# Performance work log

Measured on AMD Instinct MI355X. Metric: run time of the kernel, lower is better.

Reference implementation:

```python
import jax, jax.numpy as jnp
import numpy as np

PAD_VAL = -10000.0


def setup_inputs() -> dict:
    key = jax.random.key(0)
    k1, k2 = jax.random.split(key)
    B, C, H, W = 16, 3, 256, 256
    predicted = jax.random.normal(k1, (B, C, H, W), dtype=jnp.float32)
    ground_truth = jax.random.normal(k2, (B, C, H, W), dtype=jnp.float32)
    return {"predicted": predicted, "ground_truth": ground_truth, "nh": 5, "nw": 5}


def reference(predicted, ground_truth, nh, nw):
    # Faithful to torch: ConstantPad2d((v_pad, v_pad, h_pad, h_pad)) pads
    # W by v_pad = nh//2 and H by h_pad = nw//2 (symmetric when nh == nw).
    v_pad = nh // 2
    h_pad = nw // 2
    B, C, H, W = ground_truth.shape
    gt_pad = jnp.pad(
        ground_truth,
        ((0, 0), (0, 0), (h_pad, h_pad), (v_pad, v_pad)),
        constant_values=PAD_VAL,
    )
    # nh*nw shifted views of the padded ground truth: [B, C, H, W, nh*nw]
    refs = jnp.stack(
        [gt_pad[:, :, i:i + H, j:j + W] for i in range(nh) for j in range(nw)],
        axis=-1,
    )
    # L1 distance over channels for each neighbor shift: [B, H, W, nh*nw]
    norms = jnp.sum(jnp.abs(refs - predicted[..., None]), axis=1)
    # min over neighborhood, then mean over batch/spatial
    return jnp.mean(jnp.min(norms, axis=-1))
```

## Files before the change

kernel.cpp:

```cpp
#include <hip/hip_runtime.h>
#include <math.h>

#define PAD_VAL (-10000.0f)

constexpr int Cc = 3, Hh = 256, Ww = 256, Bb = 16;
constexpr int TW = 64;
constexpr int TH = 16;
constexpr int LDSH = TH + 4;
constexpr int LDSW = 76;
constexpr int F4_PER_ROW = 18;
constexpr int NSLOT = Cc * LDSH * F4_PER_ROW;
constexpr int NTHR  = 128;
constexpr int NBLK  = (Ww / TW) * (Hh / TH) * Bb;


__global__ __launch_bounds__(NTHR) void nnloss_main(
    const float* __restrict__ pred, const float* __restrict__ gt,
    float* __restrict__ partial)
{
    __shared__ float sh[Cc][LDSH][LDSW];
    __shared__ float wsum[2];

    const int bx = blockIdx.x, by = blockIdx.y, b = blockIdx.z;
    const int cbase = bx * TW, rbase = by * TH;
    const int tid = threadIdx.x;
    const size_t base = (size_t)b * Cc * Hh * Ww;

    const int gx  = tid & 15;
    const int ty  = tid >> 4;
    const int pr0 = 2 * ty;
    const int w0  = cbase + 4 * gx;
    const int r0  = rbase + pr0;

    float p[Cc][2][4];
#pragma unroll
    for (int ch = 0; ch < Cc; ++ch)
#pragma unroll
        for (int rr = 0; rr < 2; ++rr) {
            float4 a = *reinterpret_cast<const float4*>(
                &pred[base + ((size_t)ch * Hh + r0 + rr) * Ww + w0]);
            p[ch][rr][0] = a.x; p[ch][rr][1] = a.y;
            p[ch][rr][2] = a.z; p[ch][rr][3] = a.w;
        }

#pragma unroll
    for (int it = 0; it < 9; ++it) {
        int s = tid + it * NTHR;
        if (s < NSLOT) {
            int ch  = s / (LDSH * F4_PER_ROW);
            int rem = s - ch * (LDSH * F4_PER_ROW);
            int lr  = rem / F4_PER_ROW;
            int lc4 = rem - lr * F4_PER_ROW;
            int r   = rbase + lr - 2;
            int c0  = cbase + lc4 * 4 - 4;
            float4 v = make_float4(PAD_VAL, PAD_VAL, PAD_VAL, PAD_VAL);
            if (((unsigned)r < (unsigned)Hh) & ((unsigned)c0 < (unsigned)Ww))
                v = *reinterpret_cast<const float4*>(
                    &gt[base + ((size_t)ch * Hh + r) * Ww + c0]);
            *reinterpret_cast<float4*>(&sh[ch][lr][lc4 * 4]) = v;
        }
    }
    __syncthreads();

    float best[2][4];
#pragma unroll
    for (int rr = 0; rr < 2; ++rr)
#pragma unroll
        for (int px = 0; px < 4; ++px) best[rr][px] = 3.0e38f;

#pragma unroll
    for (int dr = 0; dr < 6; ++dr) {
        float wr[Cc][12];
#pragma unroll
        for (int ch = 0; ch < Cc; ++ch) {
            const float4* q = reinterpret_cast<const float4*>(&sh[ch][pr0 + dr][4 * gx]);
            float4 q0 = q[0], q1 = q[1], q2 = q[2];
            wr[ch][0] = q0.x; wr[ch][1]  = q0.y; wr[ch][2]  = q0.z; wr[ch][3]  = q0.w;
            wr[ch][4] = q1.x; wr[ch][5]  = q1.y; wr[ch][6]  = q1.z; wr[ch][7]  = q1.w;
            wr[ch][8] = q2.x; wr[ch][9]  = q2.y; wr[ch][10] = q2.z; wr[ch][11] = q2.w;
        }
#pragma unroll
        for (int rr = 0; rr < 2; ++rr) {
            if ((rr == 0 && dr <= 4) || (rr == 1 && dr >= 1)) {
#pragma unroll
                for (int dj = 0; dj < 5; ++dj)
#pragma unroll
                    for (int px = 0; px < 4; ++px) {
                        float s = fabsf(wr[0][px + dj + 2] - p[0][rr][px])
                                + fabsf(wr[1][px + dj + 2] - p[1][rr][px])
                                + fabsf(wr[2][px + dj + 2] - p[2][rr][px]);
                        best[rr][px] = fminf(best[rr][px], s);
                    }
            }
        }
    }

    float t = ((best[0][0] + best[0][1]) + (best[0][2] + best[0][3]))
            + ((best[1][0] + best[1][1]) + (best[1][2] + best[1][3]));
#pragma unroll
    for (int off = 32; off; off >>= 1) t += __shfl_down(t, off, 64);
    if ((tid & 63) == 0) wsum[tid >> 6] = t;
    __syncthreads();
    if (tid == 0) {
        int pid = (blockIdx.z * gridDim.y + blockIdx.y) * gridDim.x + blockIdx.x;
        partial[pid] = wsum[0] + wsum[1];
    }
}

__global__ __launch_bounds__(256) void nnloss_reduce(
    const float* __restrict__ partial, int n, float* __restrict__ out)
{
    __shared__ float ws[4];
    float t = 0.0f;
    for (int i = threadIdx.x; i < n; i += 256) t += partial[i];
#pragma unroll
    for (int off = 32; off; off >>= 1) t += __shfl_down(t, off, 64);
    if ((threadIdx.x & 63) == 0) ws[threadIdx.x >> 6] = t;
    __syncthreads();
    if (threadIdx.x == 0)
        out[0] = ((ws[0] + ws[1]) + (ws[2] + ws[3]))
               * (1.0f / ((float)Bb * (float)Hh * (float)Ww));
}

extern "C" void kernel_launch(void* const* d_in, const int* in_sizes, int n_in,
                              void* d_out, int out_size, void* d_ws, size_t ws_size,
                              hipStream_t stream) {
    const float* pred = (const float*)d_in[0];
    const float* gt   = (const float*)d_in[1];
    float* out     = (float*)d_out;
    float* partial = (float*)d_ws;

    dim3 grid(Ww / TW, Hh / TH, Bb);
    nnloss_main<<<grid, NTHR, 0, stream>>>(pred, gt, partial);
    nnloss_reduce<<<1, 256, 0, stream>>>(partial, NBLK, out);
}
```

Measured before the change: 16.90 us.

## Fuse final reduction into main kernel via last-block atomics, halve tile height

Removes the separate reduction kernel launch. The last block to finish, found through per-group and global atomic counters, now sums the partials and writes the mean. The tile height drops from 16 to 8 rows, with one output row per thread, and launch bounds request 4 blocks per CU, giving more and lighter blocks. The counters live in the workspace and rely on modulo wraparound, so results are only correct if the workspace starts zeroed. Smaller tiles also reload more halo rows per block.

```diff
diff --git a/kernel.cpp b/kernel.cpp
--- a/kernel.cpp
+++ b/kernel.cpp
@@ -4,22 +4,25 @@
 #define PAD_VAL (-10000.0f)
 
 constexpr int Cc = 3, Hh = 256, Ww = 256, Bb = 16;
-constexpr int TW = 64;
-constexpr int TH = 16;
+constexpr int TW = 64, TH = 8;
 constexpr int LDSH = TH + 4;
 constexpr int LDSW = 76;
-constexpr int F4_PER_ROW = 18;
-constexpr int NSLOT = Cc * LDSH * F4_PER_ROW;
+constexpr int F4R  = 18;
+constexpr int NSLOT = Cc * LDSH * F4R;
 constexpr int NTHR  = 128;
 constexpr int NBLK  = (Ww / TW) * (Hh / TH) * Bb;
+constexpr int GRP   = 32;
+constexpr int NGRP  = NBLK / GRP;
 
 
-__global__ __launch_bounds__(NTHR) void nnloss_main(
+__global__ __launch_bounds__(NTHR, 4) void nnloss_main(
     const float* __restrict__ pred, const float* __restrict__ gt,
-    float* __restrict__ partial)
+    float* __restrict__ partial, unsigned* __restrict__ gctr,
+    unsigned* __restrict__ fctr, float* __restrict__ out)
 {
     __shared__ float sh[Cc][LDSH][LDSW];
     __shared__ float wsum[2];
+    __shared__ int lastFlag;
 
     const int bx = blockIdx.x, by = blockIdx.y, b = blockIdx.z;
     const int cbase = bx * TW, rbase = by * TH;
@@ -28,29 +31,25 @@
 
     const int gx  = tid & 15;
     const int ty  = tid >> 4;
-    const int pr0 = 2 * ty;
     const int w0  = cbase + 4 * gx;
-    const int r0  = rbase + pr0;
+    const int row = rbase + ty;
 
-    float p[Cc][2][4];
+    float p[Cc][4];
 #pragma unroll
-    for (int ch = 0; ch < Cc; ++ch)
-#pragma unroll
-        for (int rr = 0; rr < 2; ++rr) {
-            float4 a = *reinterpret_cast<const float4*>(
-                &pred[base + ((size_t)ch * Hh + r0 + rr) * Ww + w0]);
-            p[ch][rr][0] = a.x; p[ch][rr][1] = a.y;
-            p[ch][rr][2] = a.z; p[ch][rr][3] = a.w;
-        }
+    for (int ch = 0; ch < Cc; ++ch) {
+        float4 a = *reinterpret_cast<const float4*>(
+            &pred[base + ((size_t)ch * Hh + row) * Ww + w0]);
+        p[ch][0] = a.x; p[ch][1] = a.y; p[ch][2] = a.z; p[ch][3] = a.w;
+    }
 
 #pragma unroll
-    for (int it = 0; it < 9; ++it) {
+    for (int it = 0; it < 6; ++it) {
         int s = tid + it * NTHR;
         if (s < NSLOT) {
-            int ch  = s / (LDSH * F4_PER_ROW);
-            int rem = s - ch * (LDSH * F4_PER_ROW);
-            int lr  = rem / F4_PER_ROW;
-            int lc4 = rem - lr * F4_PER_ROW;
+            int ch  = s / (LDSH * F4R);
+            int rem = s - ch * (LDSH * F4R);
+            int lr  = rem / F4R;
+            int lc4 = rem - lr * F4R;
             int r   = rbase + lr - 2;
             int c0  = cbase + lc4 * 4 - 4;
             float4 v = make_float4(PAD_VAL, PAD_VAL, PAD_VAL, PAD_VAL);
@@ -62,64 +61,67 @@
     }
     __syncthreads();
 
-    float best[2][4];
+    float best[4];
 #pragma unroll
-    for (int rr = 0; rr < 2; ++rr)
-#pragma unroll
-        for (int px = 0; px < 4; ++px) best[rr][px] = 3.0e38f;
+    for (int px = 0; px < 4; ++px) best[px] = 3.0e38f;
 
 #pragma unroll
-    for (int dr = 0; dr < 6; ++dr) {
+    for (int di = 0; di < 5; ++di) {
         float wr[Cc][12];
 #pragma unroll
         for (int ch = 0; ch < Cc; ++ch) {
-            const float4* q = reinterpret_cast<const float4*>(&sh[ch][pr0 + dr][4 * gx]);
+            const float4* q = reinterpret_cast<const float4*>(&sh[ch][ty + di][4 * gx]);
             float4 q0 = q[0], q1 = q[1], q2 = q[2];
             wr[ch][0] = q0.x; wr[ch][1]  = q0.y; wr[ch][2]  = q0.z; wr[ch][3]  = q0.w;
             wr[ch][4] = q1.x; wr[ch][5]  = q1.y; wr[ch][6]  = q1.z; wr[ch][7]  = q1.w;
             wr[ch][8] = q2.x; wr[ch][9]  = q2.y; wr[ch][10] = q2.z; wr[ch][11] = q2.w;
         }
 #pragma unroll
-        for (int rr = 0; rr < 2; ++rr) {
-            if ((rr == 0 && dr <= 4) || (rr == 1 && dr >= 1)) {
+        for (int dj = 0; dj < 5; ++dj)
 #pragma unroll
-                for (int dj = 0; dj < 5; ++dj)
-#pragma unroll
-                    for (int px = 0; px < 4; ++px) {
-                        float s = fabsf(wr[0][px + dj + 2] - p[0][rr][px])
-                                + fabsf(wr[1][px + dj + 2] - p[1][rr][px])
-                                + fabsf(wr[2][px + dj + 2] - p[2][rr][px]);
-                        best[rr][px] = fminf(best[rr][px], s);
-                    }
+            for (int px = 0; px < 4; ++px) {
+                float s = fabsf(wr[0][px + dj + 2] - p[0][px])
+                        + fabsf(wr[1][px + dj + 2] - p[1][px])
+                        + fabsf(wr[2][px + dj + 2] - p[2][px]);
+                best[px] = fminf(best[px], s);
             }
-        }
     }
 
-    float t = ((best[0][0] + best[0][1]) + (best[0][2] + best[0][3]))
-            + ((best[1][0] + best[1][1]) + (best[1][2] + best[1][3]));
+    float t = (best[0] + best[1]) + (best[2] + best[3]);
 #pragma unroll
     for (int off = 32; off; off >>= 1) t += __shfl_down(t, off, 64);
     if ((tid & 63) == 0) wsum[tid >> 6] = t;
     __syncthreads();
+
+    const int pid = (blockIdx.z * gridDim.y + blockIdx.y) * gridDim.x + blockIdx.x;
+
     if (tid == 0) {
-        int pid = (blockIdx.z * gridDim.y + blockIdx.y) * gridDim.x + blockIdx.x;
         partial[pid] = wsum[0] + wsum[1];
+        __threadfence();
+        int last = 0;
+        unsigned og = atomicAdd(&gctr[pid / GRP], 1u);
+        if ((og & (GRP - 1)) == (GRP - 1)) {
+            __threadfence();
+            unsigned of = atomicAdd(fctr, 1u);
+            if ((of & (NGRP - 1)) == (NGRP - 1))
+                last = 1;
+        }
+        lastFlag = last;
     }
-}
+    __syncthreads();
 
-__global__ __launch_bounds__(256) void nnloss_reduce(
-    const float* __restrict__ partial, int n, float* __restrict__ out)
-{
-    __shared__ float ws[4];
-    float t = 0.0f;
-    for (int i = threadIdx.x; i < n; i += 256) t += partial[i];
+    if (lastFlag) {
+        __threadfence();
+        float t2 = 0.0f;
+        for (int i = tid; i < NBLK; i += NTHR) t2 += partial[i];
 #pragma unroll
-    for (int off = 32; off; off >>= 1) t += __shfl_down(t, off, 64);
-    if ((threadIdx.x & 63) == 0) ws[threadIdx.x >> 6] = t;
-    __syncthreads();
-    if (threadIdx.x == 0)
-        out[0] = ((ws[0] + ws[1]) + (ws[2] + ws[3]))
-               * (1.0f / ((float)Bb * (float)Hh * (float)Ww));
+        for (int off = 32; off; off >>= 1) t2 += __shfl_down(t2, off, 64);
+        if ((tid & 63) == 0) wsum[tid >> 6] = t2;
+        __syncthreads();
+        if (tid == 0)
+            out[0] = (wsum[0] + wsum[1])
+                   * (1.0f / ((float)Bb * (float)Hh * (float)Ww));
+    }
 }
 
 extern "C" void kernel_launch(void* const* d_in, const int* in_sizes, int n_in,
@@ -127,10 +129,12 @@
                               hipStream_t stream) {
     const float* pred = (const float*)d_in[0];
     const float* gt   = (const float*)d_in[1];
-    float* out     = (float*)d_out;
-    float* partial = (float*)d_ws;
+    float* out = (float*)d_out;
+
+    float*    partial = (float*)d_ws;
+    unsigned* gctr    = (unsigned*)d_ws + NBLK;
+    unsigned* fctr    = (unsigned*)d_ws + NBLK + NGRP;
 
     dim3 grid(Ww / TW, Hh / TH, Bb);
-    nnloss_main<<<grid, NTHR, 0, stream>>>(pred, gt, partial);
-    nnloss_reduce<<<1, 256, 0, stream>>>(partial, NBLK, out);
+    nnloss_main<<<grid, NTHR, 0, stream>>>(pred, gt, partial, gctr, fctr, out);
 }
```

Result: slower. 50.85 us (+200.9%).

## Fuse final reduction into main kernel via last-block atomic counters

Applied to the files above, without the earlier changes.

Removes the separate reduce kernel launch by having each block publish its partial sum and bump a hierarchical pair of atomic counters (per-group, then global). The block that completes the last group sums all partials and writes the mean. The intent is to save the second launch and its inter-kernel gap. In exchange it adds atomics and uses relaxed ordering with a manual waitcnt rather than release/acquire fences. The counters are never reset, so correctness relies on the modulo checks wrapping cleanly across calls.

```diff
diff --git a/kernel.cpp b/kernel.cpp
--- a/kernel.cpp
+++ b/kernel.cpp
@@ -8,18 +8,22 @@
 constexpr int TH = 16;
 constexpr int LDSH = TH + 4;
 constexpr int LDSW = 76;
-constexpr int F4_PER_ROW = 18;
-constexpr int NSLOT = Cc * LDSH * F4_PER_ROW;
+constexpr int F4R  = 18;
+constexpr int NSLOT = Cc * LDSH * F4R;
 constexpr int NTHR  = 128;
 constexpr int NBLK  = (Ww / TW) * (Hh / TH) * Bb;
+constexpr int GRP   = 32;
+constexpr int NGRP  = NBLK / GRP;
 
 
 __global__ __launch_bounds__(NTHR) void nnloss_main(
     const float* __restrict__ pred, const float* __restrict__ gt,
-    float* __restrict__ partial)
+    float* __restrict__ partial, unsigned* __restrict__ gctr,
+    unsigned* __restrict__ fctr, float* __restrict__ out)
 {
     __shared__ float sh[Cc][LDSH][LDSW];
     __shared__ float wsum[2];
+    __shared__ int lastFlag;
 
     const int bx = blockIdx.x, by = blockIdx.y, b = blockIdx.z;
     const int cbase = bx * TW, rbase = by * TH;
@@ -47,10 +51,10 @@
     for (int it = 0; it < 9; ++it) {
         int s = tid + it * NTHR;
         if (s < NSLOT) {
-            int ch  = s / (LDSH * F4_PER_ROW);
-            int rem = s - ch * (LDSH * F4_PER_ROW);
-            int lr  = rem / F4_PER_ROW;
-            int lc4 = rem - lr * F4_PER_ROW;
+            int ch  = s / (LDSH * F4R);
+            int rem = s - ch * (LDSH * F4R);
+            int lr  = rem / F4R;
+            int lc4 = rem - lr * F4R;
             int r   = rbase + lr - 2;
             int c0  = cbase + lc4 * 4 - 4;
             float4 v = make_float4(PAD_VAL, PAD_VAL, PAD_VAL, PAD_VAL);
@@ -101,25 +105,39 @@
     for (int off = 32; off; off >>= 1) t += __shfl_down(t, off, 64);
     if ((tid & 63) == 0) wsum[tid >> 6] = t;
     __syncthreads();
+
+    const int pid = (blockIdx.z * gridDim.y + blockIdx.y) * gridDim.x + blockIdx.x;
+
     if (tid == 0) {
-        int pid = (blockIdx.z * gridDim.y + blockIdx.y) * gridDim.x + blockIdx.x;
-        partial[pid] = wsum[0] + wsum[1];
+        __hip_atomic_store(&partial[pid], wsum[0] + wsum[1],
+                           __ATOMIC_RELAXED, __HIP_MEMORY_SCOPE_AGENT);
+        asm volatile("s_waitcnt vmcnt(0)" ::: "memory");
+        int last = 0;
+        unsigned og = __hip_atomic_fetch_add(&gctr[pid / GRP], 1u,
+                          __ATOMIC_RELAXED, __HIP_MEMORY_SCOPE_AGENT);
+        if ((og & (GRP - 1)) == (GRP - 1)) {
+            unsigned of = __hip_atomic_fetch_add(fctr, 1u,
+                              __ATOMIC_RELAXED, __HIP_MEMORY_SCOPE_AGENT);
+            if ((of & (NGRP - 1)) == (NGRP - 1))
+                last = 1;
+        }
+        lastFlag = last;
     }
-}
+    __syncthreads();
 
-__global__ __launch_bounds__(256) void nnloss_reduce(
-    const float* __restrict__ partial, int n, float* __restrict__ out)
-{
-    __shared__ float ws[4];
-    float t = 0.0f;
-    for (int i = threadIdx.x; i < n; i += 256) t += partial[i];
+    if (lastFlag) {
+        float t2 = 0.0f;
+        for (int i = tid; i < NBLK; i += NTHR)
+            t2 += __hip_atomic_load(&partial[i],
+                      __ATOMIC_RELAXED, __HIP_MEMORY_SCOPE_AGENT);
 #pragma unroll
-    for (int off = 32; off; off >>= 1) t += __shfl_down(t, off, 64);
-    if ((threadIdx.x & 63) == 0) ws[threadIdx.x >> 6] = t;
-    __syncthreads();
-    if (threadIdx.x == 0)
-        out[0] = ((ws[0] + ws[1]) + (ws[2] + ws[3]))
-               * (1.0f / ((float)Bb * (float)Hh * (float)Ww));
+        for (int off = 32; off; off >>= 1) t2 += __shfl_down(t2, off, 64);
+        if ((tid & 63) == 0) wsum[tid >> 6] = t2;
+        __syncthreads();
+        if (tid == 0)
+            out[0] = (wsum[0] + wsum[1])
+                   * (1.0f / ((float)Bb * (float)Hh * (float)Ww));
+    }
 }
 
 extern "C" void kernel_launch(void* const* d_in, const int* in_sizes, int n_in,
@@ -127,10 +145,12 @@
                               hipStream_t stream) {
     const float* pred = (const float*)d_in[0];
     const float* gt   = (const float*)d_in[1];
-    float* out     = (float*)d_out;
-    float* partial = (float*)d_ws;
+    float* out = (float*)d_out;
+
+    float*    partial = (float*)d_ws;
+    unsigned* gctr    = (unsigned*)((float*)d_ws + NBLK);
+    unsigned* fctr    = gctr + NGRP;
 
     dim3 grid(Ww / TW, Hh / TH, Bb);
-    nnloss_main<<<grid, NTHR, 0, stream>>>(pred, gt, partial);
-    nnloss_reduce<<<1, 256, 0, stream>>>(partial, NBLK, out);
+    nnloss_main<<<grid, NTHR, 0, stream>>>(pred, gt, partial, gctr, fctr, out);
 }
```

Result: slower. 21.91 us (+29.6%).

## Double tile height, batch halo loads before LDS stores, single-pass reduce

Applied to the files above, without the earlier changes.

Doubles the row tile to 32 with 256 threads per block, so the 4-row halo overhead per tile shrinks and the grid halves to 512 blocks. The ground-truth halo loads are now all issued into registers first and written to LDS afterwards, so global loads can be in flight together. The final reduce uses one thread per partial instead of a strided loop. In exchange it uses more LDS and more registers per block and fewer blocks in the grid, which may reduce occupancy and latency hiding.

```diff
diff --git a/kernel.cpp b/kernel.cpp
--- a/kernel.cpp
+++ b/kernel.cpp
@@ -5,13 +5,15 @@
 
 constexpr int Cc = 3, Hh = 256, Ww = 256, Bb = 16;
 constexpr int TW = 64;
-constexpr int TH = 16;
+constexpr int TH = 32;
 constexpr int LDSH = TH + 4;
 constexpr int LDSW = 76;
-constexpr int F4_PER_ROW = 18;
-constexpr int NSLOT = Cc * LDSH * F4_PER_ROW;
-constexpr int NTHR  = 128;
+constexpr int F4R  = 18;
+constexpr int NSLOT = Cc * LDSH * F4R;
+constexpr int NTHR  = 256;
+constexpr int SIT   = (NSLOT + NTHR - 1) / NTHR;
 constexpr int NBLK  = (Ww / TW) * (Hh / TH) * Bb;
+constexpr int RTHR  = 512;
 
 
 __global__ __launch_bounds__(NTHR) void nnloss_main(
@@ -19,7 +21,7 @@
     float* __restrict__ partial)
 {
     __shared__ float sh[Cc][LDSH][LDSW];
-    __shared__ float wsum[2];
+    __shared__ float wsum[NTHR / 64];
 
     const int bx = blockIdx.x, by = blockIdx.y, b = blockIdx.z;
     const int cbase = bx * TW, rbase = by * TH;
@@ -43,23 +45,30 @@
             p[ch][rr][2] = a.z; p[ch][rr][3] = a.w;
         }
 
+    float4 stg[SIT];
+    int    laddr[SIT];
 #pragma unroll
-    for (int it = 0; it < 9; ++it) {
+    for (int it = 0; it < SIT; ++it) {
         int s = tid + it * NTHR;
+        stg[it] = make_float4(PAD_VAL, PAD_VAL, PAD_VAL, PAD_VAL);
+        laddr[it] = -1;
         if (s < NSLOT) {
-            int ch  = s / (LDSH * F4_PER_ROW);
-            int rem = s - ch * (LDSH * F4_PER_ROW);
-            int lr  = rem / F4_PER_ROW;
-            int lc4 = rem - lr * F4_PER_ROW;
+            int ch  = s / (LDSH * F4R);
+            int rem = s - ch * (LDSH * F4R);
+            int lr  = rem / F4R;
+            int lc4 = rem - lr * F4R;
+            laddr[it] = (ch * LDSH + lr) * LDSW + lc4 * 4;
             int r   = rbase + lr - 2;
             int c0  = cbase + lc4 * 4 - 4;
-            float4 v = make_float4(PAD_VAL, PAD_VAL, PAD_VAL, PAD_VAL);
             if (((unsigned)r < (unsigned)Hh) & ((unsigned)c0 < (unsigned)Ww))
-                v = *reinterpret_cast<const float4*>(
+                stg[it] = *reinterpret_cast<const float4*>(
                     &gt[base + ((size_t)ch * Hh + r) * Ww + c0]);
-            *reinterpret_cast<float4*>(&sh[ch][lr][lc4 * 4]) = v;
         }
     }
+#pragma unroll
+    for (int it = 0; it < SIT; ++it)
+        if (laddr[it] >= 0)
+            *reinterpret_cast<float4*>(&((float*)sh)[laddr[it]]) = stg[it];
     __syncthreads();
 
     float best[2][4];
@@ -103,23 +112,25 @@
     __syncthreads();
     if (tid == 0) {
         int pid = (blockIdx.z * gridDim.y + blockIdx.y) * gridDim.x + blockIdx.x;
-        partial[pid] = wsum[0] + wsum[1];
+        partial[pid] = (wsum[0] + wsum[1]) + (wsum[2] + wsum[3]);
     }
 }
 
-__global__ __launch_bounds__(256) void nnloss_reduce(
-    const float* __restrict__ partial, int n, float* __restrict__ out)
+__global__ __launch_bounds__(RTHR) void nnloss_reduce(
+    const float* __restrict__ partial, float* __restrict__ out)
 {
-    __shared__ float ws[4];
-    float t = 0.0f;
-    for (int i = threadIdx.x; i < n; i += 256) t += partial[i];
+    __shared__ float ws[RTHR / 64];
+    float t = (threadIdx.x < NBLK) ? partial[threadIdx.x] : 0.0f;
 #pragma unroll
     for (int off = 32; off; off >>= 1) t += __shfl_down(t, off, 64);
     if ((threadIdx.x & 63) == 0) ws[threadIdx.x >> 6] = t;
     __syncthreads();
-    if (threadIdx.x == 0)
-        out[0] = ((ws[0] + ws[1]) + (ws[2] + ws[3]))
-               * (1.0f / ((float)Bb * (float)Hh * (float)Ww));
+    if (threadIdx.x == 0) {
+        float s = 0.0f;
+#pragma unroll
+        for (int i = 0; i < RTHR / 64; ++i) s += ws[i];
+        out[0] = s * (1.0f / ((float)Bb * (float)Hh * (float)Ww));
+    }
 }
 
 extern "C" void kernel_launch(void* const* d_in, const int* in_sizes, int n_in,
@@ -132,5 +143,5 @@
 
     dim3 grid(Ww / TW, Hh / TH, Bb);
     nnloss_main<<<grid, NTHR, 0, stream>>>(pred, gt, partial);
-    nnloss_reduce<<<1, 256, 0, stream>>>(partial, NBLK, out);
+    nnloss_reduce<<<1, RTHR, 0, stream>>>(partial, out);
 }
```

Measured after the change: 15.54 us. 1.09x faster.
